# Performance work log

Measured on AMD Instinct MI355X. Metric: run time of the kernel, lower is better.

The kernel has to match this reference:

```python
import jax, jax.numpy as jnp
import numpy as np

N_NODES = 50000
N_EDGES = 1_000_000
D_IN = 64
HID = 64
N_GRAPHS = 128


def setup_inputs() -> dict:
    key = jax.random.key(0)
    ks = jax.random.split(key, 12)
    s = 1.0 / np.sqrt(HID)
    x = jax.random.normal(ks[0], (N_NODES, D_IN), dtype=jnp.float32)
    edge_index = jax.random.randint(ks[1], (2, N_EDGES), 0, N_NODES, dtype=jnp.int32)
    # every graph id occupied, sorted (like PyG batch vector)
    batch_index = (jnp.arange(N_NODES, dtype=jnp.int32) * N_GRAPHS) // N_NODES
    return {
        "x": x,
        "Wl0": jax.random.normal(ks[2], (HID, D_IN), jnp.float32) * s,
        "Wr0": jax.random.normal(ks[3], (HID, D_IN), jnp.float32) * s,
        "bl0": jax.random.normal(ks[4], (HID,), jnp.float32) * s,
        "Wl": jax.random.normal(ks[5], (HID, HID), jnp.float32) * s,
        "Wr": jax.random.normal(ks[6], (HID, HID), jnp.float32) * s,
        "bl": jax.random.normal(ks[7], (HID,), jnp.float32) * s,
        "W1": jax.random.normal(ks[8], (HID, HID), jnp.float32) * s,
        "b1": jax.random.normal(ks[9], (HID,), jnp.float32) * s,
        "W2": jax.random.normal(ks[10], (3, HID), jnp.float32) * s,
        "b2": jax.random.normal(ks[11], (3,), jnp.float32) * s,
        "edge_index": edge_index,
        "batch_index": batch_index,
    }


def _sage_conv(x, Wl, Wr, bl, src, dst, n_nodes):
    # PyG SAGEConv (aggr='mean'): out = lin_l(mean_{j in N(i)} x_j) + lin_r(x_i)
    msgs = jnp.take(x, src, axis=0)                               # [E, D] gather
    agg = jax.ops.segment_sum(msgs, dst, num_segments=n_nodes)    # [N, D] scatter-add
    deg = jax.ops.segment_sum(jnp.ones((src.shape[0],), x.dtype), dst, num_segments=n_nodes)
    mean = agg / jnp.clip(deg, 1.0)[:, None]
    return mean @ Wl.T + bl + x @ Wr.T


def reference(x, Wl0, Wr0, bl0, Wl, Wr, bl, W1, b1, W2, b2, edge_index, batch_index):
    src, dst = edge_index[0], edge_index[1]
    n = x.shape[0]
    h = jnp.tanh(_sage_conv(x, Wl0, Wr0, bl0, src, dst, n))
    # same SAGEConv instance reused 3 times
    for _ in range(3):
        h = jnp.tanh(_sage_conv(h, Wl, Wr, bl, src, dst, n))
    pooled = jax.ops.segment_max(h, batch_index, num_segments=N_GRAPHS)  # [G, H]
    # same lin1 reused 3 times
    g = pooled
    for _ in range(3):
        g = jnp.tanh(g @ W1.T + b1)
    return g @ W2.T + b2
```

## Files before the change

### kernel.cpp

```cpp
#include <hip/hip_runtime.h>
#include <math.h>

#define NT 256

typedef unsigned short ushort_t;
typedef unsigned int uint_t;
typedef __attribute__((ext_vector_type(8))) short bf16x8;
typedef __attribute__((ext_vector_type(4))) float f32x4;

__device__ __forceinline__ int rli(int v, int l) {
    return __builtin_amdgcn_readlane(v, l);
}
__device__ __forceinline__ int imax(int a, int b) { return a > b ? a : b; }

__device__ __forceinline__ ushort_t f2bf_rne(float f) {
    uint_t u = __float_as_uint(f);
    uint_t r = u + 0x7FFF + ((u >> 16) & 1);
    return (ushort_t)(r >> 16);
}
__device__ __forceinline__ float bf2f(ushort_t b) {
    return __uint_as_float(((uint_t)b) << 16);
}
__device__ __forceinline__ float rlf(float v, int l) {
    return __int_as_float(__builtin_amdgcn_readlane(__float_as_int(v), l));
}


__global__ void zero_i32(int* __restrict__ p, int n) {
    int t = blockIdx.x * blockDim.x + threadIdx.x;
    if (t < n) p[t] = 0;
}

__global__ void hist_dst(int* __restrict__ cnt, const int* __restrict__ dst, int n_edges) {
    int e = blockIdx.x * blockDim.x + threadIdx.x;
    if (e < n_edges) atomicAdd(&cnt[dst[e]], 1);
}

__global__ void scan_blocks(const int* __restrict__ cnt, int* __restrict__ bsum, int n) {
    __shared__ int s[NT];
    int i = blockIdx.x * NT + threadIdx.x;
    s[threadIdx.x] = (i < n) ? cnt[i] : 0;
    __syncthreads();
    for (int off = NT / 2; off > 0; off >>= 1) {
        if (threadIdx.x < off) s[threadIdx.x] += s[threadIdx.x + off];
        __syncthreads();
    }
    if (threadIdx.x == 0) bsum[blockIdx.x] = s[0];
}

__global__ void scan_bsum(const int* __restrict__ bsum, int* __restrict__ boff,
                          int nb, int* __restrict__ row_off, int n) {
    __shared__ int s[1024];
    int tid = threadIdx.x;
    int v = (tid < nb) ? bsum[tid] : 0;
    s[tid] = v;
    __syncthreads();
    for (int off = 1; off < 1024; off <<= 1) {
        int t = (tid >= off) ? s[tid - off] : 0;
        __syncthreads();
        s[tid] += t;
        __syncthreads();
    }
    if (tid < nb) boff[tid] = s[tid] - v;
    if (tid == nb - 1) row_off[n] = s[tid];
}

__global__ void scan_final(const int* __restrict__ cnt, const int* __restrict__ boff,
                           int* __restrict__ row_off, int* __restrict__ cursor, int n) {
    __shared__ int s[NT];
    int i = blockIdx.x * NT + threadIdx.x;
    int v = (i < n) ? cnt[i] : 0;
    s[threadIdx.x] = v;
    __syncthreads();
    for (int off = 1; off < NT; off <<= 1) {
        int t = (threadIdx.x >= off) ? s[threadIdx.x - off] : 0;
        __syncthreads();
        s[threadIdx.x] += t;
        __syncthreads();
    }
    if (i < n) {
        int ex = boff[blockIdx.x] + s[threadIdx.x] - v;
        row_off[i] = ex;
        cursor[i] = ex;
    }
}

__global__ void edge_scatter(int* __restrict__ csr_src, int* __restrict__ cursor,
                             const int* __restrict__ src, const int* __restrict__ dst,
                             int n_edges) {
    int e = blockIdx.x * blockDim.x + threadIdx.x;
    if (e < n_edges) {
        int p = atomicAdd(&cursor[dst[e]], 1);
        csr_src[p] = src[e];
    }
}


__global__ void f2bf_kern(ushort_t* __restrict__ o, const float* __restrict__ in, int n) {
    int t = blockIdx.x * blockDim.x + threadIdx.x;
    if (t < n) o[t] = f2bf_rne(in[t]);
}

__global__ void pack_w(ushort_t* __restrict__ packed, const float* __restrict__ Wl,
                       const float* __restrict__ Wr) {
    int t = blockIdx.x * blockDim.x + threadIdx.x;
    if (t < 8192) {
        int i = t & 7;
        int lane = (t >> 3) & 63;
        int nt = (t >> 9) & 3;
        int ks = t >> 11;
        int k = ks * 32 + ((lane >> 4) << 3) + i;
        int f = nt * 16 + (lane & 15);
        float w = (k < 64) ? Wl[f * 64 + k] : Wr[f * 64 + (k - 64)];
        packed[t] = f2bf_rne(w);
    }
}


__global__ void pool_init(float* __restrict__ pooled, int n) {
    int t = blockIdx.x * blockDim.x + threadIdx.x;
    if (t < n) pooled[t] = -INFINITY;
}

__device__ __forceinline__ void atomicMaxFloat(float* addr, float value) {
    if (value >= 0.0f)
        atomicMax((int*)addr, __float_as_int(value));
    else
        atomicMin((unsigned int*)addr, (unsigned int)__float_as_int(value));
}

__global__ __launch_bounds__(NT, 8) void sage_layer(
    ushort_t* __restrict__ out_bf, float* __restrict__ pooled,
    const ushort_t* __restrict__ hb_in,
    const int* __restrict__ row_off, const int* __restrict__ csr_src,
    const int* __restrict__ batch,
    const ushort_t* __restrict__ pw,
    const float* __restrict__ bl,
    int n_nodes, int do_pool) {
    __shared__ ushort_t A[32 * 136];
    int tid = threadIdx.x;
    int lane = tid & 63;
    int v = tid >> 6;
    int g0 = blockIdx.x * 32 + v * 8;

    int roidx = g0 + (lane < 9 ? lane : 8);
    if (roidx > n_nodes) roidx = n_nodes;
    int ro = row_off[roidx];

#pragma unroll
    for (int n = 0; n < 8; ++n) {
        int g = g0 + n;
        int row = v * 8 + n;
        if (g < n_nodes) {
            int b = rli(ro, n);
            int e_ = rli(ro, n + 1);
            int d = e_ - b;
            float mean = 0.f;
            if (d <= 64) {
                int idx = csr_src[b + (lane < d ? lane : imax(d - 1, 0))];
                float a0 = 0.f, a1 = 0.f;
                for (int j = 0; j < d; j += 8) {
                    int mm1 = d - 1;
                    int s0 = rli(idx, j);
                    int s1 = rli(idx, j + 1 < d ? j + 1 : mm1);
                    int s2 = rli(idx, j + 2 < d ? j + 2 : mm1);
                    int s3 = rli(idx, j + 3 < d ? j + 3 : mm1);
                    int s4 = rli(idx, j + 4 < d ? j + 4 : mm1);
                    int s5 = rli(idx, j + 5 < d ? j + 5 : mm1);
                    int s6 = rli(idx, j + 6 < d ? j + 6 : mm1);
                    int s7 = rli(idx, j + 7 < d ? j + 7 : mm1);
                    float v0 = bf2f(hb_in[(s0 << 6) + lane]);
                    float v1 = bf2f(hb_in[(s1 << 6) + lane]);
                    float v2 = bf2f(hb_in[(s2 << 6) + lane]);
                    float v3 = bf2f(hb_in[(s3 << 6) + lane]);
                    float v4 = bf2f(hb_in[(s4 << 6) + lane]);
                    float v5 = bf2f(hb_in[(s5 << 6) + lane]);
                    float v6 = bf2f(hb_in[(s6 << 6) + lane]);
                    float v7 = bf2f(hb_in[(s7 << 6) + lane]);
                    a0 += v0;
                    a1 += (j + 1 < d) ? v1 : 0.f;
                    a0 += (j + 2 < d) ? v2 : 0.f;
                    a1 += (j + 3 < d) ? v3 : 0.f;
                    a0 += (j + 4 < d) ? v4 : 0.f;
                    a1 += (j + 5 < d) ? v5 : 0.f;
                    a0 += (j + 6 < d) ? v6 : 0.f;
                    a1 += (j + 7 < d) ? v7 : 0.f;
                }
                mean = (a0 + a1) * (1.0f / (float)imax(d, 1));
            } else {
                float aa = 0.f;
                for (int cb = b; cb < e_; cb += 64) {
                    int m = e_ - cb; if (m > 64) m = 64;
                    int lidx = cb + (lane < m ? lane : m - 1);
                    int idx = csr_src[lidx];
                    for (int j = 0; j < m; ++j)
                        aa += bf2f(hb_in[(rli(idx, j) << 6) + lane]);
                }
                mean = aa * (1.0f / (float)imax(d, 1));
            }
            A[row * 136 + lane] = f2bf_rne(mean);
            A[row * 136 + 64 + lane] = hb_in[(size_t)g * 64 + lane];
        } else {
            A[row * 136 + lane] = 0;
            A[row * 136 + 64 + lane] = 0;
        }
    }
    __syncthreads();

    int rowtile = v >> 1;
    int a_row = rowtile * 16 + (lane & 15);
    int kbase = (lane >> 4) << 3;
#pragma unroll
    for (int p = 0; p < 2; ++p) {
        int nt = (v & 1) * 2 + p;
        f32x4 acc = {0.f, 0.f, 0.f, 0.f};
#pragma unroll
        for (int ks = 0; ks < 4; ++ks) {
            bf16x8 af = *reinterpret_cast<const bf16x8*>(&A[a_row * 136 + ks * 32 + kbase]);
            bf16x8 bf = *reinterpret_cast<const bf16x8*>(&pw[(((ks << 2) + nt) * 64 + lane) << 3]);
            acc = __builtin_amdgcn_mfma_f32_16x16x32_bf16(af, bf, acc, 0, 0, 0);
        }
        int c = nt * 16 + (lane & 15);
        float bias = bl[c];
        int rbase = blockIdx.x * 32 + rowtile * 16 + ((lane >> 4) << 2);
#pragma unroll
        for (int j = 0; j < 4; ++j) {
            int g = rbase + j;
            if (g < n_nodes) {
                float o = tanhf(acc[j] + bias);
                if (do_pool) {
                    atomicMaxFloat(&pooled[(size_t)batch[g] * 64 + c], o);
                } else {
                    out_bf[(size_t)g * 64 + c] = f2bf_rne(o);
                }
            }
        }
    }
}

__global__ void head(float* __restrict__ out, const float* __restrict__ pooled,
                     const float* __restrict__ W1, const float* __restrict__ b1,
                     const float* __restrict__ W2, const float* __restrict__ b2) {
    __shared__ float W1T[64][64];
    int tid = threadIdx.x;
    for (int t = tid; t < 4096; t += NT) {
        int f = t >> 6, k = t & 63;
        W1T[k][f] = W1[t];
    }
    __syncthreads();

    int lane = tid & 63;
    int g = blockIdx.x * (NT >> 6) + (tid >> 6);
    float v = pooled[(size_t)g * 64 + lane];
    float bias = b1[lane];
#pragma unroll
    for (int it = 0; it < 3; ++it) {
        float acc = bias;
#pragma unroll
        for (int k = 0; k < 64; ++k) {
            acc += rlf(v, k) * W1T[k][lane];
        }
        v = tanhf(acc);
    }
#pragma unroll
    for (int j = 0; j < 3; ++j) {
        float p = v * W2[j * 64 + lane];
#pragma unroll
        for (int off = 32; off >= 1; off >>= 1) p += __shfl_xor(p, off);
        if (lane == 0) out[g * 3 + j] = p + b2[j];
    }
}


extern "C" void kernel_launch(void* const* d_in, const int* in_sizes, int n_in,
                              void* d_out, int out_size, void* d_ws, size_t ws_size,
                              hipStream_t stream) {
    const float* x   = (const float*)d_in[0];
    const float* Wl0 = (const float*)d_in[1];
    const float* Wr0 = (const float*)d_in[2];
    const float* bl0 = (const float*)d_in[3];
    const float* Wl  = (const float*)d_in[4];
    const float* Wr  = (const float*)d_in[5];
    const float* bl  = (const float*)d_in[6];
    const float* W1  = (const float*)d_in[7];
    const float* b1  = (const float*)d_in[8];
    const float* W2  = (const float*)d_in[9];
    const float* b2  = (const float*)d_in[10];
    const int* ei    = (const int*)d_in[11];
    const int* batch = (const int*)d_in[12];

    int n_nodes = in_sizes[0] / 64;
    int n_edges = in_sizes[11] / 2;
    const int* src = ei;
    const int* dst = ei + n_edges;

    int nb = (n_nodes + NT - 1) / NT;
    size_t nfeat = (size_t)n_nodes * 64;

    int* csr_src  = (int*)d_ws;
    int* row_off  = csr_src + n_edges;
    int* cursor   = row_off + (n_nodes + 1);
    int* cnt      = cursor + n_nodes;
    int* bsum     = cnt + n_nodes;
    int* boff     = bsum + nb;
    float* pooled = (float*)(boff + nb);
    ushort_t* pw0 = (ushort_t*)(pooled + 128 * 64);
    ushort_t* pw  = pw0 + 8192;
    ushort_t* bfX = pw + 8192;
    ushort_t* bfA = bfX + nfeat;
    ushort_t* bfB = bfA + nfeat;

    int eblk = (n_edges + NT - 1) / NT;
    int sage_blk = (n_nodes + 31) / 32;

    zero_i32<<<nb, NT, 0, stream>>>(cnt, n_nodes);
    hist_dst<<<eblk, NT, 0, stream>>>(cnt, dst, n_edges);
    scan_blocks<<<nb, NT, 0, stream>>>(cnt, bsum, n_nodes);
    scan_bsum<<<1, 1024, 0, stream>>>(bsum, boff, nb, row_off, n_nodes);
    scan_final<<<nb, NT, 0, stream>>>(cnt, boff, row_off, cursor, n_nodes);
    edge_scatter<<<eblk, NT, 0, stream>>>(csr_src, cursor, src, dst, n_edges);

    f2bf_kern<<<(int)((nfeat + NT - 1) / NT), NT, 0, stream>>>(bfX, x, (int)nfeat);
    pack_w<<<32, NT, 0, stream>>>(pw0, Wl0, Wr0);
    pack_w<<<32, NT, 0, stream>>>(pw, Wl, Wr);
    pool_init<<<(128 * 64 + NT - 1) / NT, NT, 0, stream>>>(pooled, 128 * 64);

    sage_layer<<<sage_blk, NT, 0, stream>>>(bfA, pooled, bfX, row_off, csr_src,
                                            batch, pw0, bl0, n_nodes, 0);
    sage_layer<<<sage_blk, NT, 0, stream>>>(bfB, pooled, bfA, row_off, csr_src,
                                            batch, pw, bl, n_nodes, 0);
    sage_layer<<<sage_blk, NT, 0, stream>>>(bfA, pooled, bfB, row_off, csr_src,
                                            batch, pw, bl, n_nodes, 0);
    sage_layer<<<sage_blk, NT, 0, stream>>>(bfB, pooled, bfA, row_off, csr_src,
                                            batch, pw, bl, n_nodes, 1);

    head<<<32, NT, 0, stream>>>((float*)d_out, pooled, W1, b1, W2, b2);
}
```

Before: 396.6 us.

## Interleave two nodes' neighbor gathers per wave and shrink sage blocks to 16 rows

The SAGE layer kernel now processes nodes in pairs. Each wave issues the 8-wide neighbor row gathers for two nodes together, giving up to 16 outstanding loads per wave instead of 8 to better hide gather latency. The block shrinks from 256 to 128 threads covering 16 rows, so each of the two waves computes two MFMA column tiles of a single 16-row tile. This adds register pressure, and a pair falls back to the serial slow path if either node has degree above 64.

```diff
diff --git a/kernel.cpp b/kernel.cpp
--- a/kernel.cpp
+++ b/kernel.cpp
@@ -2,6 +2,7 @@
 #include <math.h>
 
 #define NT 256
+#define NTS 128
 
 typedef unsigned short ushort_t;
 typedef unsigned int uint_t;
@@ -129,7 +130,7 @@
         atomicMin((unsigned int*)addr, (unsigned int)__float_as_int(value));
 }
 
-__global__ __launch_bounds__(NT, 8) void sage_layer(
+__global__ __launch_bounds__(NTS, 8) void sage_layer(
     ushort_t* __restrict__ out_bf, float* __restrict__ pooled,
     const ushort_t* __restrict__ hb_in,
     const int* __restrict__ row_off, const int* __restrict__ csr_src,
@@ -137,82 +138,121 @@
     const ushort_t* __restrict__ pw,
     const float* __restrict__ bl,
     int n_nodes, int do_pool) {
-    __shared__ ushort_t A[32 * 136];
+    __shared__ ushort_t A[16 * 136];
     int tid = threadIdx.x;
     int lane = tid & 63;
     int v = tid >> 6;
-    int g0 = blockIdx.x * 32 + v * 8;
+    int g0 = blockIdx.x * 16 + v * 8;
 
     int roidx = g0 + (lane < 9 ? lane : 8);
     if (roidx > n_nodes) roidx = n_nodes;
     int ro = row_off[roidx];
 
 #pragma unroll
-    for (int n = 0; n < 8; ++n) {
-        int g = g0 + n;
-        int row = v * 8 + n;
-        if (g < n_nodes) {
-            int b = rli(ro, n);
-            int e_ = rli(ro, n + 1);
-            int d = e_ - b;
-            float mean = 0.f;
-            if (d <= 64) {
-                int idx = csr_src[b + (lane < d ? lane : imax(d - 1, 0))];
-                float a0 = 0.f, a1 = 0.f;
-                for (int j = 0; j < d; j += 8) {
-                    int mm1 = d - 1;
-                    int s0 = rli(idx, j);
-                    int s1 = rli(idx, j + 1 < d ? j + 1 : mm1);
-                    int s2 = rli(idx, j + 2 < d ? j + 2 : mm1);
-                    int s3 = rli(idx, j + 3 < d ? j + 3 : mm1);
-                    int s4 = rli(idx, j + 4 < d ? j + 4 : mm1);
-                    int s5 = rli(idx, j + 5 < d ? j + 5 : mm1);
-                    int s6 = rli(idx, j + 6 < d ? j + 6 : mm1);
-                    int s7 = rli(idx, j + 7 < d ? j + 7 : mm1);
-                    float v0 = bf2f(hb_in[(s0 << 6) + lane]);
-                    float v1 = bf2f(hb_in[(s1 << 6) + lane]);
-                    float v2 = bf2f(hb_in[(s2 << 6) + lane]);
-                    float v3 = bf2f(hb_in[(s3 << 6) + lane]);
-                    float v4 = bf2f(hb_in[(s4 << 6) + lane]);
-                    float v5 = bf2f(hb_in[(s5 << 6) + lane]);
-                    float v6 = bf2f(hb_in[(s6 << 6) + lane]);
-                    float v7 = bf2f(hb_in[(s7 << 6) + lane]);
-                    a0 += v0;
-                    a1 += (j + 1 < d) ? v1 : 0.f;
-                    a0 += (j + 2 < d) ? v2 : 0.f;
-                    a1 += (j + 3 < d) ? v3 : 0.f;
-                    a0 += (j + 4 < d) ? v4 : 0.f;
-                    a1 += (j + 5 < d) ? v5 : 0.f;
-                    a0 += (j + 6 < d) ? v6 : 0.f;
-                    a1 += (j + 7 < d) ? v7 : 0.f;
-                }
-                mean = (a0 + a1) * (1.0f / (float)imax(d, 1));
-            } else {
-                float aa = 0.f;
-                for (int cb = b; cb < e_; cb += 64) {
-                    int m = e_ - cb; if (m > 64) m = 64;
-                    int lidx = cb + (lane < m ? lane : m - 1);
-                    int idx = csr_src[lidx];
-                    for (int j = 0; j < m; ++j)
-                        aa += bf2f(hb_in[(rli(idx, j) << 6) + lane]);
-                }
-                mean = aa * (1.0f / (float)imax(d, 1));
+    for (int p = 0; p < 4; ++p) {
+        int nA = 2 * p, nB = 2 * p + 1;
+        int gA = g0 + nA, gB = g0 + nB;
+        int rowA = v * 8 + nA, rowB = v * 8 + nB;
+        int bA = rli(ro, nA), eA = rli(ro, nA + 1);
+        int bB = rli(ro, nB), eB = rli(ro, nB + 1);
+        int dA = eA - bA, dB = eB - bB;
+        bool okA = gA < n_nodes, okB = gB < n_nodes;
+        float meanA = 0.f, meanB = 0.f;
+
+        if (okA && okB && dA <= 64 && dB <= 64) {
+            int idxA = csr_src[bA + (lane < dA ? lane : imax(dA - 1, 0))];
+            int idxB = csr_src[bB + (lane < dB ? lane : imax(dB - 1, 0))];
+            int gmax = imax(dA, dB);
+            float aA0 = 0.f, aA1 = 0.f, aB0 = 0.f, aB1 = 0.f;
+            for (int j = 0; j < gmax; j += 8) {
+                float vA0, vA1, vA2, vA3, vA4, vA5, vA6, vA7;
+                float vB0, vB1, vB2, vB3, vB4, vB5, vB6, vB7;
+                bool doA = j < dA, doB = j < dB;
+                if (doA) {
+                    int mm = dA - 1;
+                    vA0 = bf2f(hb_in[(rli(idxA, j) << 6) + lane]);
+                    vA1 = bf2f(hb_in[(rli(idxA, j + 1 < dA ? j + 1 : mm) << 6) + lane]);
+                    vA2 = bf2f(hb_in[(rli(idxA, j + 2 < dA ? j + 2 : mm) << 6) + lane]);
+                    vA3 = bf2f(hb_in[(rli(idxA, j + 3 < dA ? j + 3 : mm) << 6) + lane]);
+                    vA4 = bf2f(hb_in[(rli(idxA, j + 4 < dA ? j + 4 : mm) << 6) + lane]);
+                    vA5 = bf2f(hb_in[(rli(idxA, j + 5 < dA ? j + 5 : mm) << 6) + lane]);
+                    vA6 = bf2f(hb_in[(rli(idxA, j + 6 < dA ? j + 6 : mm) << 6) + lane]);
+                    vA7 = bf2f(hb_in[(rli(idxA, j + 7 < dA ? j + 7 : mm) << 6) + lane]);
+                }
+                if (doB) {
+                    int mm = dB - 1;
+                    vB0 = bf2f(hb_in[(rli(idxB, j) << 6) + lane]);
+                    vB1 = bf2f(hb_in[(rli(idxB, j + 1 < dB ? j + 1 : mm) << 6) + lane]);
+                    vB2 = bf2f(hb_in[(rli(idxB, j + 2 < dB ? j + 2 : mm) << 6) + lane]);
+                    vB3 = bf2f(hb_in[(rli(idxB, j + 3 < dB ? j + 3 : mm) << 6) + lane]);
+                    vB4 = bf2f(hb_in[(rli(idxB, j + 4 < dB ? j + 4 : mm) << 6) + lane]);
+                    vB5 = bf2f(hb_in[(rli(idxB, j + 5 < dB ? j + 5 : mm) << 6) + lane]);
+                    vB6 = bf2f(hb_in[(rli(idxB, j + 6 < dB ? j + 6 : mm) << 6) + lane]);
+                    vB7 = bf2f(hb_in[(rli(idxB, j + 7 < dB ? j + 7 : mm) << 6) + lane]);
+                }
+                if (doA) {
+                    aA0 += vA0;
+                    aA1 += (j + 1 < dA) ? vA1 : 0.f;
+                    aA0 += (j + 2 < dA) ? vA2 : 0.f;
+                    aA1 += (j + 3 < dA) ? vA3 : 0.f;
+                    aA0 += (j + 4 < dA) ? vA4 : 0.f;
+                    aA1 += (j + 5 < dA) ? vA5 : 0.f;
+                    aA0 += (j + 6 < dA) ? vA6 : 0.f;
+                    aA1 += (j + 7 < dA) ? vA7 : 0.f;
+                }
+                if (doB) {
+                    aB0 += vB0;
+                    aB1 += (j + 1 < dB) ? vB1 : 0.f;
+                    aB0 += (j + 2 < dB) ? vB2 : 0.f;
+                    aB1 += (j + 3 < dB) ? vB3 : 0.f;
+                    aB0 += (j + 4 < dB) ? vB4 : 0.f;
+                    aB1 += (j + 5 < dB) ? vB5 : 0.f;
+                    aB0 += (j + 6 < dB) ? vB6 : 0.f;
+                    aB1 += (j + 7 < dB) ? vB7 : 0.f;
+                }
             }
-            A[row * 136 + lane] = f2bf_rne(mean);
-            A[row * 136 + 64 + lane] = hb_in[(size_t)g * 64 + lane];
+            meanA = (aA0 + aA1) * (1.0f / (float)imax(dA, 1));
+            meanB = (aB0 + aB1) * (1.0f / (float)imax(dB, 1));
         } else {
-            A[row * 136 + lane] = 0;
-            A[row * 136 + 64 + lane] = 0;
-        }
-    }
-    __syncthreads();
-
-    int rowtile = v >> 1;
-    int a_row = rowtile * 16 + (lane & 15);
+#define SLOW_NODE(MEAN, OK, B, E, D)                                          \
+            if (OK) {                                                         \
+                float aa = 0.f;                                               \
+                for (int cb = (B); cb < (E); cb += 64) {                      \
+                    int m = (E) - cb; if (m > 64) m = 64;                     \
+                    int lidx = cb + (lane < m ? lane : m - 1);                \
+                    int idx = csr_src[lidx];                                  \
+                    for (int j = 0; j < m; ++j)                               \
+                        aa += bf2f(hb_in[(rli(idx, j) << 6) + lane]);         \
+                }                                                             \
+                MEAN = aa * (1.0f / (float)imax((D), 1));                     \
+            }
+            SLOW_NODE(meanA, okA, bA, eA, dA)
+            SLOW_NODE(meanB, okB, bB, eB, dB)
+#undef SLOW_NODE
+        }
+
+        if (okA) {
+            A[rowA * 136 + lane] = f2bf_rne(meanA);
+            A[rowA * 136 + 64 + lane] = hb_in[((size_t)gA << 6) + lane];
+        } else {
+            A[rowA * 136 + lane] = 0;
+            A[rowA * 136 + 64 + lane] = 0;
+        }
+        if (okB) {
+            A[rowB * 136 + lane] = f2bf_rne(meanB);
+            A[rowB * 136 + 64 + lane] = hb_in[((size_t)gB << 6) + lane];
+        } else {
+            A[rowB * 136 + lane] = 0;
+            A[rowB * 136 + 64 + lane] = 0;
+        }
+    }
+    __syncthreads();
+
+    int a_row = lane & 15;
     int kbase = (lane >> 4) << 3;
 #pragma unroll
     for (int p = 0; p < 2; ++p) {
-        int nt = (v & 1) * 2 + p;
+        int nt = v * 2 + p;
         f32x4 acc = {0.f, 0.f, 0.f, 0.f};
 #pragma unroll
         for (int ks = 0; ks < 4; ++ks) {
@@ -222,7 +262,7 @@
         }
         int c = nt * 16 + (lane & 15);
         float bias = bl[c];
-        int rbase = blockIdx.x * 32 + rowtile * 16 + ((lane >> 4) << 2);
+        int rbase = blockIdx.x * 16 + ((lane >> 4) << 2);
 #pragma unroll
         for (int j = 0; j < 4; ++j) {
             int g = rbase + j;
@@ -311,7 +351,7 @@
     ushort_t* bfB = bfA + nfeat;
 
     int eblk = (n_edges + NT - 1) / NT;
-    int sage_blk = (n_nodes + 31) / 32;
+    int sage_blk = (n_nodes + 15) / 16;
 
     zero_i32<<<nb, NT, 0, stream>>>(cnt, n_nodes);
     hist_dst<<<eblk, NT, 0, stream>>>(cnt, dst, n_edges);
@@ -325,14 +365,14 @@
     pack_w<<<32, NT, 0, stream>>>(pw, Wl, Wr);
     pool_init<<<(128 * 64 + NT - 1) / NT, NT, 0, stream>>>(pooled, 128 * 64);
 
-    sage_layer<<<sage_blk, NT, 0, stream>>>(bfA, pooled, bfX, row_off, csr_src,
-                                            batch, pw0, bl0, n_nodes, 0);
-    sage_layer<<<sage_blk, NT, 0, stream>>>(bfB, pooled, bfA, row_off, csr_src,
-                                            batch, pw, bl, n_nodes, 0);
-    sage_layer<<<sage_blk, NT, 0, stream>>>(bfA, pooled, bfB, row_off, csr_src,
-                                            batch, pw, bl, n_nodes, 0);
-    sage_layer<<<sage_blk, NT, 0, stream>>>(bfB, pooled, bfA, row_off, csr_src,
-                                            batch, pw, bl, n_nodes, 1);
+    sage_layer<<<sage_blk, NTS, 0, stream>>>(bfA, pooled, bfX, row_off, csr_src,
+                                             batch, pw0, bl0, n_nodes, 0);
+    sage_layer<<<sage_blk, NTS, 0, stream>>>(bfB, pooled, bfA, row_off, csr_src,
+                                             batch, pw, bl, n_nodes, 0);
+    sage_layer<<<sage_blk, NTS, 0, stream>>>(bfA, pooled, bfB, row_off, csr_src,
+                                             batch, pw, bl, n_nodes, 0);
+    sage_layer<<<sage_blk, NTS, 0, stream>>>(bfB, pooled, bfA, row_off, csr_src,
+                                             batch, pw, bl, n_nodes, 1);
 
     head<<<32, NT, 0, stream>>>((float*)d_out, pooled, W1, b1, W2, b2);
 }
```

After: 390.0 us. Within noise of the previous version (-1.7%).

## Pipeline neighbor gathers through async global-to-LDS ring buffer in SAGE layer

Applied to the files above, without the earlier changes.

Rewrites the mean-aggregation gather in the SAGE layer so that neighbor rows are fetched with global_load_lds async copies into a double-banked per-wave LDS ring. The next node's loads are issued while the current node's rows are summed, and fixed vmcnt waits throttle the pipeline. Edge indices for the block are preloaded into registers. Nodes with more than 32 neighbors, or whose edges fall outside the preloaded 256-edge window, are recomputed with a plain serial fallback. The block shrinks to 128 threads and 16 nodes to make room for the ring in LDS and to raise occupancy. The intent is to hide gather latency, at the cost of always issuing 32 padded loads per node and of fragile hand-written waitcnt ordering.

```diff
diff --git a/kernel.cpp b/kernel.cpp
--- a/kernel.cpp
+++ b/kernel.cpp
@@ -2,6 +2,7 @@
 #include <math.h>
 
 #define NT 256
+#define NTS 128
 
 typedef unsigned short ushort_t;
 typedef unsigned int uint_t;
@@ -12,6 +13,7 @@
     return __builtin_amdgcn_readlane(v, l);
 }
 __device__ __forceinline__ int imax(int a, int b) { return a > b ? a : b; }
+__device__ __forceinline__ int imin(int a, int b) { return a < b ? a : b; }
 
 __device__ __forceinline__ ushort_t f2bf_rne(float f) {
     uint_t u = __float_as_uint(f);
@@ -23,6 +25,20 @@
 }
 __device__ __forceinline__ float rlf(float v, int l) {
     return __int_as_float(__builtin_amdgcn_readlane(__float_as_int(v), l));
+}
+
+__device__ __forceinline__ void async_copy4(const void* g, void* l) {
+    __builtin_amdgcn_global_load_lds(
+        (__attribute__((address_space(1))) unsigned int*)(unsigned long long)g,
+        (__attribute__((address_space(3))) unsigned int*)l,
+        4, 0, 0);
+}
+
+__device__ __forceinline__ int selidx(int pos, int e0, int e1, int e2, int e3) {
+    int l = pos & 63;
+    int r0 = rli(e0, l), r1 = rli(e1, l), r2 = rli(e2, l), r3 = rli(e3, l);
+    int j = pos >> 6;
+    return j == 0 ? r0 : (j == 1 ? r1 : (j == 2 ? r2 : r3));
 }
 
 
@@ -129,90 +145,122 @@
         atomicMin((unsigned int*)addr, (unsigned int)__float_as_int(value));
 }
 
-__global__ __launch_bounds__(NT, 8) void sage_layer(
+__global__ __launch_bounds__(NTS, 8) void sage_layer(
     ushort_t* __restrict__ out_bf, float* __restrict__ pooled,
     const ushort_t* __restrict__ hb_in,
     const int* __restrict__ row_off, const int* __restrict__ csr_src,
     const int* __restrict__ batch,
     const ushort_t* __restrict__ pw,
     const float* __restrict__ bl,
-    int n_nodes, int do_pool) {
-    __shared__ ushort_t A[32 * 136];
+    int n_nodes, int n_edges, int do_pool) {
+    __shared__ ushort_t A[16 * 136];
+    __shared__ uint_t RING[2][2048];
     int tid = threadIdx.x;
     int lane = tid & 63;
     int v = tid >> 6;
-    int g0 = blockIdx.x * 32 + v * 8;
-
-    int roidx = g0 + (lane < 9 ? lane : 8);
-    if (roidx > n_nodes) roidx = n_nodes;
+    int g0 = blockIdx.x * 16 + v * 8;
+    int l31 = lane & 31;
+
+    int roidx = imin(g0 + imin(lane, 8), n_nodes);
     int ro = row_off[roidx];
-
-#pragma unroll
+    int eb = rli(ro, 0);
+    int emax = n_edges - 1;
+
+    int ev0 = csr_src[imin(eb + lane, emax)];
+    int ev1 = csr_src[imin(eb + 64 + lane, emax)];
+    int ev2 = csr_src[imin(eb + 128 + lane, emax)];
+    int ev3 = csr_src[imin(eb + 192 + lane, emax)];
+
     for (int n = 0; n < 8; ++n) {
         int g = g0 + n;
         int row = v * 8 + n;
-        if (g < n_nodes) {
-            int b = rli(ro, n);
-            int e_ = rli(ro, n + 1);
-            int d = e_ - b;
-            float mean = 0.f;
-            if (d <= 64) {
-                int idx = csr_src[b + (lane < d ? lane : imax(d - 1, 0))];
-                float a0 = 0.f, a1 = 0.f;
-                for (int j = 0; j < d; j += 8) {
-                    int mm1 = d - 1;
-                    int s0 = rli(idx, j);
-                    int s1 = rli(idx, j + 1 < d ? j + 1 : mm1);
-                    int s2 = rli(idx, j + 2 < d ? j + 2 : mm1);
-                    int s3 = rli(idx, j + 3 < d ? j + 3 : mm1);
-                    int s4 = rli(idx, j + 4 < d ? j + 4 : mm1);
-                    int s5 = rli(idx, j + 5 < d ? j + 5 : mm1);
-                    int s6 = rli(idx, j + 6 < d ? j + 6 : mm1);
-                    int s7 = rli(idx, j + 7 < d ? j + 7 : mm1);
-                    float v0 = bf2f(hb_in[(s0 << 6) + lane]);
-                    float v1 = bf2f(hb_in[(s1 << 6) + lane]);
-                    float v2 = bf2f(hb_in[(s2 << 6) + lane]);
-                    float v3 = bf2f(hb_in[(s3 << 6) + lane]);
-                    float v4 = bf2f(hb_in[(s4 << 6) + lane]);
-                    float v5 = bf2f(hb_in[(s5 << 6) + lane]);
-                    float v6 = bf2f(hb_in[(s6 << 6) + lane]);
-                    float v7 = bf2f(hb_in[(s7 << 6) + lane]);
-                    a0 += v0;
-                    a1 += (j + 1 < d) ? v1 : 0.f;
-                    a0 += (j + 2 < d) ? v2 : 0.f;
-                    a1 += (j + 3 < d) ? v3 : 0.f;
-                    a0 += (j + 4 < d) ? v4 : 0.f;
-                    a1 += (j + 5 < d) ? v5 : 0.f;
-                    a0 += (j + 6 < d) ? v6 : 0.f;
-                    a1 += (j + 7 < d) ? v7 : 0.f;
-                }
-                mean = (a0 + a1) * (1.0f / (float)imax(d, 1));
-            } else {
-                float aa = 0.f;
-                for (int cb = b; cb < e_; cb += 64) {
-                    int m = e_ - cb; if (m > 64) m = 64;
-                    int lidx = cb + (lane < m ? lane : m - 1);
-                    int idx = csr_src[lidx];
-                    for (int j = 0; j < m; ++j)
-                        aa += bf2f(hb_in[(rli(idx, j) << 6) + lane]);
-                }
-                mean = aa * (1.0f / (float)imax(d, 1));
+        uint_t hw = 0;
+        if (g < n_nodes)
+            hw = *(const uint_t*)&hb_in[((size_t)g << 6) + 2 * l31];
+        *(uint_t*)&A[row * 136 + 64 + 2 * l31] = hw;
+    }
+    asm volatile("s_waitcnt vmcnt(0)" ::: "memory");
+
+#define ISSUE(BN, DN, BANK, S)                                                \
+    {                                                                         \
+        int dc_ = imin((DN), 32);                                             \
+        int lastp_ = imax(dc_ - 1, 0);                                        \
+        int p0_ = imin(2 * (S), lastp_);                                      \
+        int p1_ = imin(2 * (S) + 1, lastp_);                                  \
+        int pos0_ = imin((BN) - eb + p0_, 255);                               \
+        int pos1_ = imin((BN) - eb + p1_, 255);                               \
+        int iA_ = selidx(pos0_, ev0, ev1, ev2, ev3);                          \
+        int iB_ = selidx(pos1_, ev0, ev1, ev2, ev3);                          \
+        int isel_ = (lane < 32) ? iA_ : iB_;                                  \
+        const char* src_ = (const char*)hb_in +                               \
+            (((size_t)(unsigned)isel_) << 7) + ((size_t)l31 << 2);            \
+        async_copy4(src_, &RING[v][(BANK) * 1024 + (S) * 64]);                \
+    }
+
+    {
+        int b0 = rli(ro, 0), d0v = rli(ro, 1) - b0;
+        for (int s = 0; s < 16; ++s) ISSUE(b0, d0v, 0, s);
+        int b1 = rli(ro, 1), d1v = rli(ro, 2) - b1;
+        for (int s = 0; s < 16; ++s) ISSUE(b1, d1v, 1, s);
+    }
+
+    for (int n = 0; n < 8; ++n) {
+        int bn = rli(ro, n);
+        int dn = rli(ro, n + 1) - bn;
+        int m = imin(n + 2, 7);
+        int bm = rli(ro, m);
+        int dm = rli(ro, m + 1) - bm;
+        int bank = n & 1;
+        int dc = imin(dn, 32);
+        float accLo = 0.f, accHi = 0.f;
+        for (int s = 0; s < 16; ++s) {
+            asm volatile("s_waitcnt vmcnt(31)" ::: "memory");
+            const uint_t* sl = &RING[v][bank * 1024 + s * 64];
+            uint_t aw = sl[l31];
+            uint_t bw = sl[32 + l31];
+            float fa = (2 * s < dc) ? 1.f : 0.f;
+            float fb = (2 * s + 1 < dc) ? 1.f : 0.f;
+            accLo += fa * __uint_as_float(aw << 16);
+            accHi += fa * __uint_as_float(aw & 0xffff0000u);
+            accLo += fb * __uint_as_float(bw << 16);
+            accHi += fb * __uint_as_float(bw & 0xffff0000u);
+            ISSUE(bm, dm, bank, s);
+        }
+        float inv = 1.0f / (float)imax(dn, 1);
+        uint_t mw = (uint_t)f2bf_rne(accLo * inv) |
+                    ((uint_t)f2bf_rne(accHi * inv) << 16);
+        *(uint_t*)&A[(v * 8 + n) * 136 + 2 * l31] = mw;
+    }
+    asm volatile("s_waitcnt vmcnt(0)" ::: "memory");
+
+    for (int n = 0; n < 8; ++n) {
+        int bn = rli(ro, n);
+        int en = rli(ro, n + 1);
+        int dn = en - bn;
+        bool flag = (dn > 32) || ((bn - eb + imin(dn, 32)) > 256);
+        int g = g0 + n;
+        if (flag && g < n_nodes) {
+            float aLo = 0.f, aHi = 0.f;
+            for (int e = bn; e < en; ++e) {
+                int idx = csr_src[e];
+                uint_t hw = *(const uint_t*)&hb_in[((size_t)idx << 6) + 2 * l31];
+                aLo += __uint_as_float(hw << 16);
+                aHi += __uint_as_float(hw & 0xffff0000u);
             }
-            A[row * 136 + lane] = f2bf_rne(mean);
-            A[row * 136 + 64 + lane] = hb_in[(size_t)g * 64 + lane];
-        } else {
-            A[row * 136 + lane] = 0;
-            A[row * 136 + 64 + lane] = 0;
-        }
-    }
-    __syncthreads();
-
-    int rowtile = v >> 1;
-    int a_row = rowtile * 16 + (lane & 15);
+            float inv = 1.0f / (float)imax(dn, 1);
+            uint_t mw = (uint_t)f2bf_rne(aLo * inv) |
+                        ((uint_t)f2bf_rne(aHi * inv) << 16);
+            *(uint_t*)&A[(v * 8 + n) * 136 + 2 * l31] = mw;
+        }
+    }
+#undef ISSUE
+    __syncthreads();
+
+    int a_row = lane & 15;
     int kbase = (lane >> 4) << 3;
 #pragma unroll
     for (int p = 0; p < 2; ++p) {
-        int nt = (v & 1) * 2 + p;
+        int nt = v * 2 + p;
         f32x4 acc = {0.f, 0.f, 0.f, 0.f};
 #pragma unroll
         for (int ks = 0; ks < 4; ++ks) {
@@ -222,7 +270,7 @@
         }
         int c = nt * 16 + (lane & 15);
         float bias = bl[c];
-        int rbase = blockIdx.x * 32 + rowtile * 16 + ((lane >> 4) << 2);
+        int rbase = blockIdx.x * 16 + ((lane >> 4) << 2);
 #pragma unroll
         for (int j = 0; j < 4; ++j) {
             int g = rbase + j;
@@ -311,7 +359,7 @@
     ushort_t* bfB = bfA + nfeat;
 
     int eblk = (n_edges + NT - 1) / NT;
-    int sage_blk = (n_nodes + 31) / 32;
+    int sage_blk = (n_nodes + 15) / 16;
 
     zero_i32<<<nb, NT, 0, stream>>>(cnt, n_nodes);
     hist_dst<<<eblk, NT, 0, stream>>>(cnt, dst, n_edges);
@@ -325,14 +373,14 @@
     pack_w<<<32, NT, 0, stream>>>(pw, Wl, Wr);
     pool_init<<<(128 * 64 + NT - 1) / NT, NT, 0, stream>>>(pooled, 128 * 64);
 
-    sage_layer<<<sage_blk, NT, 0, stream>>>(bfA, pooled, bfX, row_off, csr_src,
-                                            batch, pw0, bl0, n_nodes, 0);
-    sage_layer<<<sage_blk, NT, 0, stream>>>(bfB, pooled, bfA, row_off, csr_src,
-                                            batch, pw, bl, n_nodes, 0);
-    sage_layer<<<sage_blk, NT, 0, stream>>>(bfA, pooled, bfB, row_off, csr_src,
-                                            batch, pw, bl, n_nodes, 0);
-    sage_layer<<<sage_blk, NT, 0, stream>>>(bfB, pooled, bfA, row_off, csr_src,
-                                            batch, pw, bl, n_nodes, 1);
+    sage_layer<<<sage_blk, NTS, 0, stream>>>(bfA, pooled, bfX, row_off, csr_src,
+                                             batch, pw0, bl0, n_nodes, n_edges, 0);
+    sage_layer<<<sage_blk, NTS, 0, stream>>>(bfB, pooled, bfA, row_off, csr_src,
+                                             batch, pw, bl, n_nodes, n_edges, 0);
+    sage_layer<<<sage_blk, NTS, 0, stream>>>(bfA, pooled, bfB, row_off, csr_src,
+                                             batch, pw, bl, n_nodes, n_edges, 0);
+    sage_layer<<<sage_blk, NTS, 0, stream>>>(bfB, pooled, bfA, row_off, csr_src,
+                                             batch, pw, bl, n_nodes, n_edges, 1);
 
     head<<<32, NT, 0, stream>>>((float*)d_out, pooled, W1, b1, W2, b2);
 }
```

After: 635.5 us. 60.2% more time.

## Gather two neighbor rows per wave with 32-bit loads and shrink SAGE blocks

Applied to the files above, without the earlier changes.

The aggregation loop now splits each wave into two half-waves. Each half loads a different neighbor row as 32-bit words (two bf16 features per lane), and the halves are combined with a cross-lane xor shuffle. This cuts the number of load instructions per edge and raises the bytes moved per load. The SAGE kernel also goes from 256-thread blocks covering 32 nodes to 128-thread blocks covering 16 nodes, which doubles the block count and reshapes how the MFMA tiles map onto waves. In exchange it adds masking multiplies and a shuffle reduction per node.

```diff
diff --git a/kernel.cpp b/kernel.cpp
--- a/kernel.cpp
+++ b/kernel.cpp
@@ -2,6 +2,7 @@
 #include <math.h>
 
 #define NT 256
+#define NTS 128
 
 typedef unsigned short ushort_t;
 typedef unsigned int uint_t;
@@ -12,6 +13,7 @@
     return __builtin_amdgcn_readlane(v, l);
 }
 __device__ __forceinline__ int imax(int a, int b) { return a > b ? a : b; }
+__device__ __forceinline__ int imin(int a, int b) { return a < b ? a : b; }
 
 __device__ __forceinline__ ushort_t f2bf_rne(float f) {
     uint_t u = __float_as_uint(f);
@@ -129,7 +131,7 @@
         atomicMin((unsigned int*)addr, (unsigned int)__float_as_int(value));
 }
 
-__global__ __launch_bounds__(NT, 8) void sage_layer(
+__global__ __launch_bounds__(NTS, 8) void sage_layer(
     ushort_t* __restrict__ out_bf, float* __restrict__ pooled,
     const ushort_t* __restrict__ hb_in,
     const int* __restrict__ row_off, const int* __restrict__ csr_src,
@@ -137,82 +139,85 @@
     const ushort_t* __restrict__ pw,
     const float* __restrict__ bl,
     int n_nodes, int do_pool) {
-    __shared__ ushort_t A[32 * 136];
+    __shared__ ushort_t A[16 * 136];
     int tid = threadIdx.x;
     int lane = tid & 63;
     int v = tid >> 6;
-    int g0 = blockIdx.x * 32 + v * 8;
-
-    int roidx = g0 + (lane < 9 ? lane : 8);
-    if (roidx > n_nodes) roidx = n_nodes;
+    int g0 = blockIdx.x * 16 + v * 8;
+    int l31 = lane & 31;
+    int h = lane >> 5;
+    const uint_t* hb32 = (const uint_t*)hb_in;
+
+    int roidx = imin(g0 + imin(lane, 8), n_nodes);
     int ro = row_off[roidx];
 
 #pragma unroll
     for (int n = 0; n < 8; ++n) {
         int g = g0 + n;
         int row = v * 8 + n;
-        if (g < n_nodes) {
-            int b = rli(ro, n);
-            int e_ = rli(ro, n + 1);
-            int d = e_ - b;
-            float mean = 0.f;
-            if (d <= 64) {
-                int idx = csr_src[b + (lane < d ? lane : imax(d - 1, 0))];
-                float a0 = 0.f, a1 = 0.f;
-                for (int j = 0; j < d; j += 8) {
-                    int mm1 = d - 1;
-                    int s0 = rli(idx, j);
-                    int s1 = rli(idx, j + 1 < d ? j + 1 : mm1);
-                    int s2 = rli(idx, j + 2 < d ? j + 2 : mm1);
-                    int s3 = rli(idx, j + 3 < d ? j + 3 : mm1);
-                    int s4 = rli(idx, j + 4 < d ? j + 4 : mm1);
-                    int s5 = rli(idx, j + 5 < d ? j + 5 : mm1);
-                    int s6 = rli(idx, j + 6 < d ? j + 6 : mm1);
-                    int s7 = rli(idx, j + 7 < d ? j + 7 : mm1);
-                    float v0 = bf2f(hb_in[(s0 << 6) + lane]);
-                    float v1 = bf2f(hb_in[(s1 << 6) + lane]);
-                    float v2 = bf2f(hb_in[(s2 << 6) + lane]);
-                    float v3 = bf2f(hb_in[(s3 << 6) + lane]);
-                    float v4 = bf2f(hb_in[(s4 << 6) + lane]);
-                    float v5 = bf2f(hb_in[(s5 << 6) + lane]);
-                    float v6 = bf2f(hb_in[(s6 << 6) + lane]);
-                    float v7 = bf2f(hb_in[(s7 << 6) + lane]);
-                    a0 += v0;
-                    a1 += (j + 1 < d) ? v1 : 0.f;
-                    a0 += (j + 2 < d) ? v2 : 0.f;
-                    a1 += (j + 3 < d) ? v3 : 0.f;
-                    a0 += (j + 4 < d) ? v4 : 0.f;
-                    a1 += (j + 5 < d) ? v5 : 0.f;
-                    a0 += (j + 6 < d) ? v6 : 0.f;
-                    a1 += (j + 7 < d) ? v7 : 0.f;
+        int b = rli(ro, n);
+        int e_ = rli(ro, n + 1);
+        int d = e_ - b;
+        bool ok = g < n_nodes;
+
+        A[row * 136 + 64 + lane] = ok ? hb_in[((size_t)g << 6) + lane] : (ushort_t)0;
+
+        if (ok && d <= 64) {
+            int idx = csr_src[b + (lane < d ? lane : imax(d - 1, 0))];
+            float accLo = 0.f, accHi = 0.f;
+            for (int jj = 0; jj < d; jj += 16) {
+                uint_t w0, w1, w2, w3, w4, w5, w6, w7;
+#define LD(L, W)                                                              \
+                {                                                             \
+                    int eA = imin(jj + 2 * (L), d - 1);                       \
+                    int eB = imin(jj + 2 * (L) + 1, d - 1);                   \
+                    int iA = rli(idx, eA);                                    \
+                    int iB = rli(idx, eB);                                    \
+                    int is = (lane < 32) ? iA : iB;                           \
+                    W = hb32[((size_t)(unsigned)is << 5) + l31];              \
                 }
-                mean = (a0 + a1) * (1.0f / (float)imax(d, 1));
-            } else {
-                float aa = 0.f;
-                for (int cb = b; cb < e_; cb += 64) {
-                    int m = e_ - cb; if (m > 64) m = 64;
-                    int lidx = cb + (lane < m ? lane : m - 1);
-                    int idx = csr_src[lidx];
-                    for (int j = 0; j < m; ++j)
-                        aa += bf2f(hb_in[(rli(idx, j) << 6) + lane]);
+                LD(0, w0) LD(1, w1) LD(2, w2) LD(3, w3)
+                LD(4, w4) LD(5, w5) LD(6, w6) LD(7, w7)
+#undef LD
+#define CS(L, W)                                                              \
+                {                                                             \
+                    float f = ((jj + 2 * (L) + h) < d) ? 1.f : 0.f;           \
+                    accLo += f * __uint_as_float((W) << 16);                  \
+                    accHi += f * __uint_as_float((W) & 0xffff0000u);          \
                 }
-                mean = aa * (1.0f / (float)imax(d, 1));
+                CS(0, w0) CS(1, w1) CS(2, w2) CS(3, w3)
+                CS(4, w4) CS(5, w5) CS(6, w6) CS(7, w7)
+#undef CS
             }
-            A[row * 136 + lane] = f2bf_rne(mean);
-            A[row * 136 + 64 + lane] = hb_in[(size_t)g * 64 + lane];
+            accLo += __shfl_xor(accLo, 32);
+            accHi += __shfl_xor(accHi, 32);
+            float inv = 1.0f / (float)imax(d, 1);
+            if (lane < 32) {
+                uint_t mw = (uint_t)f2bf_rne(accLo * inv) |
+                            ((uint_t)f2bf_rne(accHi * inv) << 16);
+                *(uint_t*)&A[row * 136 + 2 * l31] = mw;
+            }
+        } else if (ok) {
+            float aa = 0.f;
+            for (int cb = b; cb < e_; cb += 64) {
+                int m = e_ - cb; if (m > 64) m = 64;
+                int lidx = cb + (lane < m ? lane : m - 1);
+                int idx2 = csr_src[lidx];
+                for (int j = 0; j < m; ++j)
+                    aa += bf2f(hb_in[((size_t)(unsigned)rli(idx2, j) << 6) + lane]);
+            }
+            A[row * 136 + lane] = f2bf_rne(aa * (1.0f / (float)imax(d, 1)));
         } else {
             A[row * 136 + lane] = 0;
-            A[row * 136 + 64 + lane] = 0;
         }
     }
     __syncthreads();
 
-    int rowtile = v >> 1;
-    int a_row = rowtile * 16 + (lane & 15);
+    int a_row = lane & 15;
     int kbase = (lane >> 4) << 3;
 #pragma unroll
     for (int p = 0; p < 2; ++p) {
-        int nt = (v & 1) * 2 + p;
+        int nt = v * 2 + p;
         f32x4 acc = {0.f, 0.f, 0.f, 0.f};
 #pragma unroll
         for (int ks = 0; ks < 4; ++ks) {
@@ -222,7 +227,7 @@
         }
         int c = nt * 16 + (lane & 15);
         float bias = bl[c];
-        int rbase = blockIdx.x * 32 + rowtile * 16 + ((lane >> 4) << 2);
+        int rbase = blockIdx.x * 16 + ((lane >> 4) << 2);
 #pragma unroll
         for (int j = 0; j < 4; ++j) {
             int g = rbase + j;
@@ -311,7 +316,7 @@
     ushort_t* bfB = bfA + nfeat;
 
     int eblk = (n_edges + NT - 1) / NT;
-    int sage_blk = (n_nodes + 31) / 32;
+    int sage_blk = (n_nodes + 15) / 16;
 
     zero_i32<<<nb, NT, 0, stream>>>(cnt, n_nodes);
     hist_dst<<<eblk, NT, 0, stream>>>(cnt, dst, n_edges);
@@ -325,14 +330,14 @@
     pack_w<<<32, NT, 0, stream>>>(pw, Wl, Wr);
     pool_init<<<(128 * 64 + NT - 1) / NT, NT, 0, stream>>>(pooled, 128 * 64);
 
-    sage_layer<<<sage_blk, NT, 0, stream>>>(bfA, pooled, bfX, row_off, csr_src,
-                                            batch, pw0, bl0, n_nodes, 0);
-    sage_layer<<<sage_blk, NT, 0, stream>>>(bfB, pooled, bfA, row_off, csr_src,
-                                            batch, pw, bl, n_nodes, 0);
-    sage_layer<<<sage_blk, NT, 0, stream>>>(bfA, pooled, bfB, row_off, csr_src,
-                                            batch, pw, bl, n_nodes, 0);
-    sage_layer<<<sage_blk, NT, 0, stream>>>(bfB, pooled, bfA, row_off, csr_src,
-                                            batch, pw, bl, n_nodes, 1);
+    sage_layer<<<sage_blk, NTS, 0, stream>>>(bfA, pooled, bfX, row_off, csr_src,
+                                             batch, pw0, bl0, n_nodes, 0);
+    sage_layer<<<sage_blk, NTS, 0, stream>>>(bfB, pooled, bfA, row_off, csr_src,
+                                             batch, pw, bl, n_nodes, 0);
+    sage_layer<<<sage_blk, NTS, 0, stream>>>(bfA, pooled, bfB, row_off, csr_src,
+                                             batch, pw, bl, n_nodes, 0);
+    sage_layer<<<sage_blk, NTS, 0, stream>>>(bfB, pooled, bfA, row_off, csr_src,
+                                             batch, pw, bl, n_nodes, 1);
 
     head<<<32, NT, 0, stream>>>((float*)d_out, pooled, W1, b1, W2, b2);
 }
```

New measurement: 399.7 us. About the same (+0.8%).
